# Kernel optimization log

Measured on AMD Instinct MI355X. Metric: run time of the kernel, lower is better.

The kernel has to match this reference:

```python
import jax, jax.numpy as jnp
import numpy as np

N_NODES = 100000
N_EDGES = 800000
IN_DIM, HID, OUT_DIM = 128, 96, 32
BN_EPS = 1e-5


def gcn_conv(x, W, b, src, dst, n):
    # PyG GCNConv: linear -> symmetric-normalized aggregation (with self-loops) -> +bias
    h = x @ W  # [N, out]
    sl = jnp.arange(n)
    s = jnp.concatenate([src, sl])
    d = jnp.concatenate([dst, sl])
    deg = jax.ops.segment_sum(jnp.ones(s.shape[0], dtype=x.dtype), d, num_segments=n)
    dinv = jnp.where(deg > 0, jax.lax.rsqrt(deg), 0.0)
    norm = dinv[s] * dinv[d]  # [E+N]
    out = jax.ops.segment_sum(norm[:, None] * h[s], d, num_segments=n)
    return out + b


def batchnorm(x, gamma, beta):
    mu = jnp.mean(x, axis=0)
    var = jnp.var(x, axis=0)
    return gamma * (x - mu) * jax.lax.rsqrt(var + BN_EPS) + beta


def setup_inputs() -> dict:
    key = jax.random.key(0)
    ks = jax.random.split(key, 8)
    glorot = lambda k, fi, fo: jax.random.normal(k, (fi, fo), jnp.float32) * np.sqrt(2.0 / (fi + fo))
    return {
        "x": jax.random.normal(ks[0], (N_NODES, IN_DIM), jnp.float32),
        "edge_index": jax.random.randint(ks[1], (2, N_EDGES), 0, N_NODES, jnp.int64),
        "W1": glorot(ks[2], IN_DIM, HID), "b1": jnp.zeros((HID,), jnp.float32),
        "W2": glorot(ks[3], HID, HID), "b2": jnp.zeros((HID,), jnp.float32),
        "W3": glorot(ks[4], HID, OUT_DIM), "b3": jnp.zeros((OUT_DIM,), jnp.float32),
        "g1": jnp.ones((HID,), jnp.float32), "be1": jnp.zeros((HID,), jnp.float32),
        "g2": jnp.ones((HID,), jnp.float32), "be2": jnp.zeros((HID,), jnp.float32),
    }


def reference(x, edge_index, W1, b1, W2, b2, W3, b3, g1, be1, g2, be2):
    src, dst = edge_index[0], edge_index[1]
    n = x.shape[0]
    h = gcn_conv(x, W1, b1, src, dst, n)
    h = jax.nn.relu(batchnorm(h, g1, be1))  # dropout is identity in eval
    h = gcn_conv(h, W2, b2, src, dst, n)
    h = jax.nn.relu(batchnorm(h, g2, be2))
    h = gcn_conv(h, W3, b3, src, dst, n)
    return jax.nn.log_softmax(h, axis=-1)
```

## Files before the change

### kernel.cpp

```cpp
#include <hip/hip_runtime.h>
#include <hip/hip_fp16.h>
#include <cstddef>

#define NN 100000
#define NE 800000
#define DIN 128
#define HID 96
#define DOUT 32
static constexpr float BN_EPS = 1e-5f;
#define SCAN_NB ((NN + 255) / 256)

typedef unsigned short u16;
typedef unsigned int u32;

__device__ __forceinline__ float b2f(u32 lo16) {
    union { u32 u; float f; } c; c.u = lo16 << 16; return c.f;
}
__device__ __forceinline__ u16 f2b(float f) {
    union { float f; u32 u; } c; c.f = f;
    return (u16)((c.u + 0x7FFFu + ((c.u >> 16) & 1u)) >> 16);
}
__device__ __forceinline__ u32 pack_edge(int s, float w) {
    __half h = __float2half(w);
    return ((u32)s << 15) | (u32)__half_as_ushort(h);
}
__device__ __forceinline__ int edge_src(u32 pk) { return (int)(pk >> 15); }
__device__ __forceinline__ float edge_wt(u32 pk) {
    return __half2float(__ushort_as_half((u16)(pk & 0x7FFFu)));
}


__global__ void k_init(int* __restrict__ deg) {
    int i = blockIdx.x * 256 + threadIdx.x;
    if (i < NN) deg[i] = 0;
}

__global__ __launch_bounds__(256) void k_scan1(const int* __restrict__ deg,
                                               int* __restrict__ row_start,
                                               int* __restrict__ blksum,
                                               float* __restrict__ dinv) {
    __shared__ int lds[256];
    int t = threadIdx.x;
    int i = blockIdx.x * 256 + t;
    int v = (i < NN) ? deg[i] : 0;
    if (i < NN) dinv[i] = rsqrtf((float)(v + 1));
    lds[t] = v;
    __syncthreads();
#pragma unroll
    for (int off = 1; off < 256; off <<= 1) {
        int add = (t >= off) ? lds[t - off] : 0;
        __syncthreads();
        lds[t] += add;
        __syncthreads();
    }
    if (i < NN) row_start[i] = lds[t] - v;
    if (t == 255) blksum[blockIdx.x] = lds[255];
}

__global__ __launch_bounds__(512) void k_scan2(int* __restrict__ blksum,
                                               int* __restrict__ row_start,
                                               float* __restrict__ meta) {
    __shared__ int lds[512];
    int t = threadIdx.x;
    if (t < 384) meta[t] = 0.f;
    int v = (t < SCAN_NB) ? blksum[t] : 0;
    lds[t] = v;
    __syncthreads();
#pragma unroll
    for (int off = 1; off < 512; off <<= 1) {
        int add = (t >= off) ? lds[t - off] : 0;
        __syncthreads();
        lds[t] += add;
        __syncthreads();
    }
    if (t < SCAN_NB) blksum[t] = lds[t] - v;
    if (t == 511) row_start[NN] = lds[511];
}

__global__ __launch_bounds__(256) void k_scan3(int* __restrict__ row_start,
                                               const int* __restrict__ blksum) {
    int i = blockIdx.x * 256 + threadIdx.x;
    if (i < NN) row_start[i] += blksum[blockIdx.x];
}

__global__ void k_scatter(const int* __restrict__ src, const int* __restrict__ dst,
                          const int* __restrict__ row_start,
                          const int* __restrict__ rank,
                          const float* __restrict__ dinv,
                          u32* __restrict__ ewt) {
    int e = blockIdx.x * blockDim.x + threadIdx.x;
    if (e < NE) {
        int d = dst[e];
        int p = row_start[d] + rank[e];
        int s = src[e];
        ewt[p] = pack_edge(s, dinv[s]);
    }
}

template <int KD, int ND, bool FUSE, typename XT>
__device__ __forceinline__ void gemm_body(int bid, const XT* __restrict__ X,
                                          const float* __restrict__ W,
                                          u16* __restrict__ Z,
                                          const float* __restrict__ bnA,
                                          const float* __restrict__ bnC, int M) {
    constexpr int BK = 32;
    constexpr int CT = 16;
    constexpr int CPT = ND / CT;
    constexpr int RPT = 8;
    constexpr int XS = 132;
    __shared__ float Xs[BK * XS];
    __shared__ float Ws[BK * ND];
    __shared__ float As[KD], Cs[KD];

    int tid = threadIdx.x;
    if (FUSE && tid < KD) { As[tid] = bnA[tid]; Cs[tid] = bnC[tid]; }
    int row0 = bid * 128;
    int ct = tid % CT, rt = tid / CT;
    float acc[RPT][CPT];
#pragma unroll
    for (int r = 0; r < RPT; ++r)
#pragma unroll
        for (int c = 0; c < CPT; ++c) acc[r][c] = 0.f;

    for (int k0 = 0; k0 < KD; k0 += BK) {
        __syncthreads();
        if constexpr (sizeof(XT) == 4) {
#pragma unroll
            for (int pass = 0; pass < 4; ++pass) {
                int r = pass * 32 + (tid >> 3);
                int kq = (tid & 7) * 4;
                int grow = row0 + r;
                float4 v = make_float4(0.f, 0.f, 0.f, 0.f);
                if (grow < M) v = *(const float4*)&X[(size_t)grow * KD + k0 + kq];
                if (FUSE) {
                    v.x = fmaxf(fmaf(As[k0 + kq + 0], v.x, Cs[k0 + kq + 0]), 0.f);
                    v.y = fmaxf(fmaf(As[k0 + kq + 1], v.y, Cs[k0 + kq + 1]), 0.f);
                    v.z = fmaxf(fmaf(As[k0 + kq + 2], v.z, Cs[k0 + kq + 2]), 0.f);
                    v.w = fmaxf(fmaf(As[k0 + kq + 3], v.w, Cs[k0 + kq + 3]), 0.f);
                }
                Xs[(kq + 0) * XS + r] = v.x;
                Xs[(kq + 1) * XS + r] = v.y;
                Xs[(kq + 2) * XS + r] = v.z;
                Xs[(kq + 3) * XS + r] = v.w;
            }
        } else {
#pragma unroll
            for (int pass = 0; pass < 2; ++pass) {
                int r = pass * 64 + (tid >> 2);
                int kq = (tid & 3) * 8;
                int grow = row0 + r;
                uint4 v = make_uint4(0, 0, 0, 0);
                if (grow < M) v = *(const uint4*)&X[(size_t)grow * KD + k0 + kq];
                u32 w[4] = {v.x, v.y, v.z, v.w};
#pragma unroll
                for (int q = 0; q < 4; ++q) {
                    float lo = b2f(w[q] & 0xFFFFu);
                    float hi = b2f(w[q] >> 16);
                    if (FUSE) {
                        lo = fmaxf(fmaf(As[k0 + kq + 2 * q + 0], lo, Cs[k0 + kq + 2 * q + 0]), 0.f);
                        hi = fmaxf(fmaf(As[k0 + kq + 2 * q + 1], hi, Cs[k0 + kq + 2 * q + 1]), 0.f);
                    }
                    Xs[(kq + 2 * q + 0) * XS + r] = lo;
                    Xs[(kq + 2 * q + 1) * XS + r] = hi;
                }
            }
        }
#pragma unroll
        for (int f = tid; f < BK * ND / 4; f += 256) {
            int kk = f / (ND / 4);
            int c4 = (f % (ND / 4)) * 4;
            *(float4*)&Ws[kk * ND + c4] = *(const float4*)&W[(size_t)(k0 + kk) * ND + c4];
        }
        __syncthreads();
#pragma unroll
        for (int kk = 0; kk < BK; ++kk) {
            float4 x0 = *(const float4*)&Xs[kk * XS + rt * 8];
            float4 x1 = *(const float4*)&Xs[kk * XS + rt * 8 + 4];
            float xr[RPT] = {x0.x, x0.y, x0.z, x0.w, x1.x, x1.y, x1.z, x1.w};
            float wc[CPT];
#pragma unroll
            for (int c = 0; c < CPT; ++c) wc[c] = Ws[kk * ND + ct * CPT + c];
#pragma unroll
            for (int r = 0; r < RPT; ++r)
#pragma unroll
                for (int c = 0; c < CPT; ++c) acc[r][c] = fmaf(xr[r], wc[c], acc[r][c]);
        }
    }
#pragma unroll
    for (int r = 0; r < RPT; ++r) {
        int grow = row0 + rt * RPT + r;
        if (grow < M) {
#pragma unroll
            for (int c = 0; c < CPT; c += 2) {
                u32 pk = (u32)f2b(acc[r][c]) | ((u32)f2b(acc[r][c + 1]) << 16);
                *(u32*)&Z[(size_t)grow * ND + ct * CPT + c] = pk;
            }
        }
    }
}

template <int KD, int ND, bool FUSE, typename XT>
__global__ __launch_bounds__(256) void k_gemm(const XT* __restrict__ X,
                                              const float* __restrict__ W,
                                              u16* __restrict__ Z,
                                              const float* __restrict__ bnA,
                                              const float* __restrict__ bnC, int M) {
    gemm_body<KD, ND, FUSE, XT>(blockIdx.x, X, W, Z, bnA, bnC, M);
}

__global__ __launch_bounds__(256) void k_gemm1_hist(const float* __restrict__ X,
                                                    const float* __restrict__ W,
                                                    u16* __restrict__ Z, int M,
                                                    int gemm_blocks,
                                                    const int* __restrict__ dst,
                                                    int* __restrict__ deg,
                                                    int* __restrict__ rank) {
    if ((int)blockIdx.x < gemm_blocks) {
        gemm_body<DIN, HID, false, float>(blockIdx.x, X, W, Z, nullptr, nullptr, M);
    } else {
        int e = ((int)blockIdx.x - gemm_blocks) * 256 + (int)threadIdx.x;
        if (e < NE) rank[e] = atomicAdd(&deg[dst[e]], 1);
    }
}

__global__ __launch_bounds__(256) void k_agg96(const u16* __restrict__ Z,
                                               u16* __restrict__ H,
                                               const float* __restrict__ bias,
                                               const int* __restrict__ row_start,
                                               const u32* __restrict__ ewt,
                                               const float* __restrict__ dinv,
                                               float* __restrict__ gsum,
                                               float* __restrict__ gsq) {
    __shared__ float ssum[96], ssq[96];
    int tid = threadIdx.x;
    if (tid < 96) { ssum[tid] = 0.f; ssq[tid] = 0.f; }
    __syncthreads();
    int wid = tid >> 6, lane = tid & 63;
    bool act = lane < 48;
    int l = act ? lane : 47;
    const u32* zu = (const u32*)Z;
    float b0 = bias[2 * l], b1 = bias[2 * l + 1];
    float lsum0 = 0.f, lsq0 = 0.f, lsum1 = 0.f, lsq1 = 0.f;
    const int stride = gridDim.x * 4;

    int n = blockIdx.x * 4 + wid;
    int e0 = 0, e1 = 0;
    u32 pr = 0;
    if (n < NN) {
        e0 = row_start[n]; e1 = row_start[n + 1];
        if (e0 + lane < e1) pr = ewt[e0 + lane];
    }
    while (n < NN) {
        int n2 = n + stride;
        int e0n = 0, e1n = 0;
        if (n2 < NN) { e0n = row_start[n2]; e1n = row_start[n2 + 1]; }

        float dn = dinv[n];
        u32 uself = zu[(size_t)n * 48 + l];
        float a0a = dn * b2f(uself & 0xFFFFu);
        float a1a = dn * b2f(uself >> 16);
        float a0b = 0.f, a1b = 0.f;

        u32 plv = pr;

        u32 prn = 0;
        if (n2 < NN && e0n + lane < e1n) prn = ewt[e0n + lane];

        int m = e1 - e0;
        if (m <= 64) {
            int K = (m + 7) >> 3;
            u32 uA[8], uB[8];
            float wA[8], wB[8];
            {
#pragma unroll
                for (int q = 0; q < 8; ++q) {
                    bool v = q < m;
                    u32 pk = __shfl(plv, v ? q : 0);
                    wA[q] = v ? edge_wt(pk) : 0.f;
                    uA[q] = zu[(size_t)edge_src(pk) * 48 + l];
                }
            }
            for (int c = 0; c < K; ++c) {
                if ((c & 1) == 0) {
                    if (c + 1 < K) {
#pragma unroll
                        for (int q = 0; q < 8; ++q) {
                            int j = (c + 1) * 8 + q;
                            bool v = j < m;
                            u32 pk = __shfl(plv, v ? j : 0);
                            wB[q] = v ? edge_wt(pk) : 0.f;
                            uB[q] = zu[(size_t)edge_src(pk) * 48 + l];
                        }
                    }
#pragma unroll
                    for (int q = 0; q < 8; q += 2) {
                        a0a = fmaf(wA[q], b2f(uA[q] & 0xFFFFu), a0a);
                        a1a = fmaf(wA[q], b2f(uA[q] >> 16), a1a);
                        a0b = fmaf(wA[q + 1], b2f(uA[q + 1] & 0xFFFFu), a0b);
                        a1b = fmaf(wA[q + 1], b2f(uA[q + 1] >> 16), a1b);
                    }
                } else {
                    if (c + 1 < K) {
#pragma unroll
                        for (int q = 0; q < 8; ++q) {
                            int j = (c + 1) * 8 + q;
                            bool v = j < m;
                            u32 pk = __shfl(plv, v ? j : 0);
                            wA[q] = v ? edge_wt(pk) : 0.f;
                            uA[q] = zu[(size_t)edge_src(pk) * 48 + l];
                        }
                    }
#pragma unroll
                    for (int q = 0; q < 8; q += 2) {
                        a0a = fmaf(wB[q], b2f(uB[q] & 0xFFFFu), a0a);
                        a1a = fmaf(wB[q], b2f(uB[q] >> 16), a1a);
                        a0b = fmaf(wB[q + 1], b2f(uB[q + 1] & 0xFFFFu), a0b);
                        a1b = fmaf(wB[q + 1], b2f(uB[q + 1] >> 16), a1b);
                    }
                }
            }
        } else {
            u32 cw = plv;
            for (int eb = e0; eb < e1; eb += 64) {
                if (eb != e0) {
                    int idx = eb + lane;
                    cw = (idx < e1) ? ewt[idx] : 0;
                }
                int mm = e1 - eb; if (mm > 64) mm = 64;
                for (int j = 0; j < mm; ++j) {
                    u32 pk = __shfl(cw, j);
                    float w = edge_wt(pk);
                    u32 u = zu[(size_t)edge_src(pk) * 48 + l];
                    a0a = fmaf(w, b2f(u & 0xFFFFu), a0a);
                    a1a = fmaf(w, b2f(u >> 16), a1a);
                }
            }
        }
        float h0 = fmaf(dn, a0a + a0b, b0);
        float h1 = fmaf(dn, a1a + a1b, b1);
        if (act) {
            u32 pk = (u32)f2b(h0) | ((u32)f2b(h1) << 16);
            ((u32*)H)[(size_t)n * 48 + l] = pk;
            lsum0 += h0; lsq0 = fmaf(h0, h0, lsq0);
            lsum1 += h1; lsq1 = fmaf(h1, h1, lsq1);
        }
        n = n2; e0 = e0n; e1 = e1n; pr = prn;
    }
    if (act) {
        atomicAdd(&ssum[2 * l], lsum0); atomicAdd(&ssq[2 * l], lsq0);
        atomicAdd(&ssum[2 * l + 1], lsum1); atomicAdd(&ssq[2 * l + 1], lsq1);
    }
    __syncthreads();
    if (tid < 96) { atomicAdd(&gsum[tid], ssum[tid]); atomicAdd(&gsq[tid], ssq[tid]); }
}

__global__ void k_bncoef(const float* __restrict__ gsum, const float* __restrict__ gsq,
                         const float* __restrict__ g, const float* __restrict__ be,
                         float* __restrict__ bnA, float* __restrict__ bnC) {
    int c = threadIdx.x;
    if (c < 96) {
        float mean = gsum[c] * (1.f / NN);
        float var = gsq[c] * (1.f / NN) - mean * mean;
        float inv = rsqrtf(var + BN_EPS);
        float a = g[c] * inv;
        bnA[c] = a;
        bnC[c] = fmaf(-a, mean, be[c]);
    }
}

__global__ __launch_bounds__(256) void k_agg32_lsm(const u16* __restrict__ Z,
                                                   float* __restrict__ Out,
                                                   const float* __restrict__ bias,
                                                   const int* __restrict__ row_start,
                                                   const u32* __restrict__ ewt,
                                                   const float* __restrict__ dinv) {
    int tid = threadIdx.x;
    int wid = tid >> 6, lane = tid & 63;
    int g = lane >> 4, sl = lane & 15;
    const u32* zu = (const u32*)Z;
    float b0 = bias[2 * sl], b1 = bias[2 * sl + 1];
    int stride = gridDim.x * 16;
    for (int n0 = (blockIdx.x * 4 + wid) * 4; n0 < NN; n0 += stride) {
        int n = n0 + g;
        bool vn = n < NN;
        float dn = vn ? dinv[n] : 0.f;
        u32 uself = vn ? zu[(size_t)n * 16 + sl] : 0;
        float a0a = dn * b2f(uself & 0xFFFFu);
        float a1a = dn * b2f(uself >> 16);
        float a0b = 0.f, a1b = 0.f;
        int e0 = vn ? row_start[n] : 0, e1 = vn ? row_start[n + 1] : 0;
        for (int eb = e0; eb < e1; eb += 16) {
            int m = e1 - eb; if (m > 16) m = 16;
            int idx = eb + sl;
            u32 plv = (idx < e1) ? ewt[idx] : 0;
            u32 u_[16]; float w_[16];
#pragma unroll
            for (int q = 0; q < 16; ++q) {
                bool v = q < m;
                u32 pk = __shfl(plv, v ? q : 0, 16);
                w_[q] = v ? edge_wt(pk) : 0.f;
                u_[q] = zu[(size_t)edge_src(pk) * 16 + sl];
            }
#pragma unroll
            for (int q = 0; q < 16; q += 2) {
                a0a = fmaf(w_[q], b2f(u_[q] & 0xFFFFu), a0a);
                a1a = fmaf(w_[q], b2f(u_[q] >> 16), a1a);
                a0b = fmaf(w_[q + 1], b2f(u_[q + 1] & 0xFFFFu), a0b);
                a1b = fmaf(w_[q + 1], b2f(u_[q + 1] >> 16), a1b);
            }
        }
        float v0 = fmaf(dn, a0a + a0b, b0);
        float v1 = fmaf(dn, a1a + a1b, b1);
        float mx = fmaxf(v0, v1);
#pragma unroll
        for (int off = 8; off; off >>= 1) mx = fmaxf(mx, __shfl_xor(mx, off, 16));
        float ex = __expf(v0 - mx) + __expf(v1 - mx);
#pragma unroll
        for (int off = 8; off; off >>= 1) ex += __shfl_xor(ex, off, 16);
        float lse = mx + __logf(ex);
        if (vn) {
            float2 o = make_float2(v0 - lse, v1 - lse);
            *(float2*)&Out[(size_t)n * 32 + 2 * sl] = o;
        }
    }
}


extern "C" void kernel_launch(void* const* d_in, const int* in_sizes, int n_in,
                              void* d_out, int out_size, void* d_ws, size_t ws_size,
                              hipStream_t stream) {
    const float* x  = (const float*)d_in[0];
    const int* ei   = (const int*)d_in[1];
    const float* W1 = (const float*)d_in[2];
    const float* b1 = (const float*)d_in[3];
    const float* W2 = (const float*)d_in[4];
    const float* b2 = (const float*)d_in[5];
    const float* W3 = (const float*)d_in[6];
    const float* b3 = (const float*)d_in[7];
    const float* g1 = (const float*)d_in[8];
    const float* be1 = (const float*)d_in[9];
    const float* g2 = (const float*)d_in[10];
    const float* be2 = (const float*)d_in[11];
    float* out = (float*)d_out;

    const int* src = ei;
    const int* dst = ei + NE;

    char* p = (char*)d_ws;
    size_t off = 0;
    auto take = [&](size_t bytes) {
        char* r = p + off;
        off = (off + bytes + 255) & ~(size_t)255;
        return r;
    };
    float* dinv      = (float*)take(NN * 4);
    int*   deg       = (int*)take(NN * 4);
    int*   row_start = (int*)take((NN + 1) * 4);
    int*   blksum    = (int*)take(SCAN_NB * 4);
    int*   rank      = (int*)take((size_t)NE * 4);
    u32*   ewt       = (u32*)take((size_t)NE * 4);
    float* meta      = (float*)take(768 * 4);
    u16*   bufA      = (u16*)take((size_t)NN * HID * 2);
    u16*   bufB      = (u16*)take((size_t)NN * HID * 2);

    float* sum1 = meta + 0,   *sq1 = meta + 96;
    float* sum2 = meta + 192, *sq2 = meta + 288;
    float* bnA1 = meta + 384, *bnC1 = meta + 480;
    float* bnA2 = meta + 576, *bnC2 = meta + 672;

    const int EB = (NE + 255) / 256;
    const int VB = (NN + 255) / 256;
    const int GB = (NN + 127) / 128;
    const int AB = 2048;

    k_init<<<VB, 256, 0, stream>>>(deg);
    k_gemm1_hist<<<GB + EB, 256, 0, stream>>>(x, W1, bufA, NN, GB, dst, deg, rank);
    k_scan1<<<SCAN_NB, 256, 0, stream>>>(deg, row_start, blksum, dinv);
    k_scan2<<<1, 512, 0, stream>>>(blksum, row_start, meta);
    k_scan3<<<SCAN_NB, 256, 0, stream>>>(row_start, blksum);
    k_scatter<<<EB, 256, 0, stream>>>(src, dst, row_start, rank, dinv, ewt);

    k_agg96<<<AB, 256, 0, stream>>>(bufA, bufB, b1, row_start, ewt, dinv, sum1, sq1);
    k_bncoef<<<1, 128, 0, stream>>>(sum1, sq1, g1, be1, bnA1, bnC1);

    k_gemm<HID, HID, true, u16><<<GB, 256, 0, stream>>>(bufB, W2, bufA, bnA1, bnC1, NN);
    k_agg96<<<AB, 256, 0, stream>>>(bufA, bufB, b2, row_start, ewt, dinv, sum2, sq2);
    k_bncoef<<<1, 128, 0, stream>>>(sum2, sq2, g2, be2, bnA2, bnC2);

    k_gemm<HID, DOUT, true, u16><<<GB, 256, 0, stream>>>(bufB, W3, bufA, bnA2, bnC2, NN);
    k_agg32_lsm<<<AB, 256, 0, stream>>>(bufA, out, b3, row_start, ewt, dinv);

    (void)in_sizes; (void)n_in; (void)out_size; (void)ws_size;
}
```

Before: 436.1 us.

## Software-pipeline GCN aggregation across nodes with 16-edge gather prefetch

Restructures the 96-wide aggregation kernel into a multi-stage pipeline. Row bounds are fetched three nodes ahead, edge words two nodes ahead, and up to 16 neighbor feature rows for the next node are gathered while the current node is accumulated, using double-buffered register arrays. Edge counts are made wave-uniform with readfirstlane, and addressing uses 32-bit byte offsets. The aim is to hide gather latency across node iterations, at the cost of higher register pressure. Nodes with more than 16 edges now do the remaining gathers serially with no prefetch.

```diff
diff --git a/kernel.cpp b/kernel.cpp
--- a/kernel.cpp
+++ b/kernel.cpp
@@ -27,6 +27,9 @@
 __device__ __forceinline__ int edge_src(u32 pk) { return (int)(pk >> 15); }
 __device__ __forceinline__ float edge_wt(u32 pk) {
     return __half2float(__ushort_as_half((u16)(pk & 0x7FFFu)));
+}
+__device__ __forceinline__ u32 ld32(const u32* __restrict__ base, u32 byteoff) {
+    return *(const u32*)((const char*)base + byteoff);
 }
 
 
@@ -238,114 +241,124 @@
     int wid = tid >> 6, lane = tid & 63;
     bool act = lane < 48;
     int l = act ? lane : 47;
+    u32 l4 = (u32)l << 2;
     const u32* zu = (const u32*)Z;
     float b0 = bias[2 * l], b1 = bias[2 * l + 1];
     float lsum0 = 0.f, lsq0 = 0.f, lsum1 = 0.f, lsq1 = 0.f;
-    const int stride = gridDim.x * 4;
-
-    int n = blockIdx.x * 4 + wid;
-    int e0 = 0, e1 = 0;
-    u32 pr = 0;
-    if (n < NN) {
-        e0 = row_start[n]; e1 = row_start[n + 1];
-        if (e0 + lane < e1) pr = ewt[e0 + lane];
-    }
-    while (n < NN) {
-        int n2 = n + stride;
-        int e0n = 0, e1n = 0;
-        if (n2 < NN) { e0n = row_start[n2]; e1n = row_start[n2 + 1]; }
-
-        float dn = dinv[n];
-        u32 uself = zu[(size_t)n * 48 + l];
-        float a0a = dn * b2f(uself & 0xFFFFu);
-        float a1a = dn * b2f(uself >> 16);
+    const int S = gridDim.x * 4;
+
+    int nA = blockIdx.x * 4 + wid;
+    int nB = nA + S, nC = nB + S, nD = nC + S;
+    int e0A = 0, e1A = 0, e0B = 0, e1B = 0, e0C = 0, e1C = 0;
+    u32 prA = 0, prB = 0;
+    u32 selfA = 0, selfB = 0;
+    float dnA = 0.f, dnB = 0.f;
+    u32 uA[16], uB[16];
+    u32 prC_ = 0; int e0D_ = 0, e1D_ = 0;
+
+    auto prefetch_rows = [&](u32 (&dst)[16], u32 pr, int m) {
+#pragma unroll
+        for (int q = 0; q < 16; ++q) {
+            if (q < m) {
+                u32 pk = __shfl(pr, q);
+                dst[q] = ld32(zu, (u32)edge_src(pk) * 192u + l4);
+            }
+        }
+    };
+
+    e0A = row_start[nA]; e1A = row_start[nA + 1];
+    if (nB < NN) { e0B = row_start[nB]; e1B = row_start[nB + 1]; }
+    if (nC < NN) { e0C = row_start[nC]; e1C = row_start[nC + 1]; }
+    if (e0A + lane < e1A) prA = ewt[e0A + lane];
+    if (nB < NN && e0B + lane < e1B) prB = ewt[e0B + lane];
+    dnA = dinv[nA];
+    selfA = ld32(zu, (u32)nA * 192u + l4);
+    prefetch_rows(uA, prA, __builtin_amdgcn_readfirstlane(e1A - e0A));
+
+    auto stage = [&](u32 (&uNxt)[16]) {
+        if (nB < NN) {
+            dnB = dinv[nB];
+            selfB = ld32(zu, (u32)nB * 192u + l4);
+            prefetch_rows(uNxt, prB, __builtin_amdgcn_readfirstlane(e1B - e0B));
+        }
+        prC_ = 0;
+        if (nC < NN && e0C + lane < e1C) prC_ = ewt[e0C + lane];
+        e0D_ = 0; e1D_ = 0;
+        if (nD < NN) { e0D_ = row_start[nD]; e1D_ = row_start[nD + 1]; }
+    };
+
+    auto compute = [&](u32 (&u)[16]) {
+        int e0s = __builtin_amdgcn_readfirstlane(e0A);
+        int e1s = __builtin_amdgcn_readfirstlane(e1A);
+        int m = e1s - e0s;
+        float a0a = dnA * b2f(selfA & 0xFFFFu);
+        float a1a = dnA * b2f(selfA >> 16);
         float a0b = 0.f, a1b = 0.f;
-
-        u32 plv = pr;
-
-        u32 prn = 0;
-        if (n2 < NN && e0n + lane < e1n) prn = ewt[e0n + lane];
-
-        int m = e1 - e0;
-        if (m <= 64) {
-            int K = (m + 7) >> 3;
-            u32 uA[8], uB[8];
-            float wA[8], wB[8];
-            {
-#pragma unroll
-                for (int q = 0; q < 8; ++q) {
-                    bool v = q < m;
-                    u32 pk = __shfl(plv, v ? q : 0);
-                    wA[q] = v ? edge_wt(pk) : 0.f;
-                    uA[q] = zu[(size_t)edge_src(pk) * 48 + l];
-                }
-            }
-            for (int c = 0; c < K; ++c) {
-                if ((c & 1) == 0) {
-                    if (c + 1 < K) {
-#pragma unroll
-                        for (int q = 0; q < 8; ++q) {
-                            int j = (c + 1) * 8 + q;
-                            bool v = j < m;
-                            u32 pk = __shfl(plv, v ? j : 0);
-                            wB[q] = v ? edge_wt(pk) : 0.f;
-                            uB[q] = zu[(size_t)edge_src(pk) * 48 + l];
-                        }
-                    }
-#pragma unroll
-                    for (int q = 0; q < 8; q += 2) {
-                        a0a = fmaf(wA[q], b2f(uA[q] & 0xFFFFu), a0a);
-                        a1a = fmaf(wA[q], b2f(uA[q] >> 16), a1a);
-                        a0b = fmaf(wA[q + 1], b2f(uA[q + 1] & 0xFFFFu), a0b);
-                        a1b = fmaf(wA[q + 1], b2f(uA[q + 1] >> 16), a1b);
-                    }
-                } else {
-                    if (c + 1 < K) {
-#pragma unroll
-                        for (int q = 0; q < 8; ++q) {
-                            int j = (c + 1) * 8 + q;
-                            bool v = j < m;
-                            u32 pk = __shfl(plv, v ? j : 0);
-                            wA[q] = v ? edge_wt(pk) : 0.f;
-                            uA[q] = zu[(size_t)edge_src(pk) * 48 + l];
-                        }
-                    }
-#pragma unroll
-                    for (int q = 0; q < 8; q += 2) {
-                        a0a = fmaf(wB[q], b2f(uB[q] & 0xFFFFu), a0a);
-                        a1a = fmaf(wB[q], b2f(uB[q] >> 16), a1a);
-                        a0b = fmaf(wB[q + 1], b2f(uB[q + 1] & 0xFFFFu), a0b);
-                        a1b = fmaf(wB[q + 1], b2f(uB[q + 1] >> 16), a1b);
-                    }
-                }
-            }
-        } else {
-            u32 cw = plv;
-            for (int eb = e0; eb < e1; eb += 64) {
-                if (eb != e0) {
-                    int idx = eb + lane;
-                    cw = (idx < e1) ? ewt[idx] : 0;
-                }
-                int mm = e1 - eb; if (mm > 64) mm = 64;
+#pragma unroll
+        for (int q = 0; q < 16; q += 2) {
+            if (q < m) {
+                u32 pk = __shfl(prA, q);
+                float w = edge_wt(pk);
+                a0a = fmaf(w, b2f(u[q] & 0xFFFFu), a0a);
+                a1a = fmaf(w, b2f(u[q] >> 16), a1a);
+            }
+            if (q + 1 < m) {
+                u32 pk = __shfl(prA, q + 1);
+                float w = edge_wt(pk);
+                a0b = fmaf(w, b2f(u[q + 1] & 0xFFFFu), a0b);
+                a1b = fmaf(w, b2f(u[q + 1] >> 16), a1b);
+            }
+        }
+        if (m > 16) {
+            int lim = m < 64 ? m : 64;
+            for (int j = 16; j < lim; ++j) {
+                u32 pk = __shfl(prA, j);
+                float w = edge_wt(pk);
+                u32 uu = ld32(zu, (u32)edge_src(pk) * 192u + l4);
+                a0a = fmaf(w, b2f(uu & 0xFFFFu), a0a);
+                a1a = fmaf(w, b2f(uu >> 16), a1a);
+            }
+            for (int eb = e0s + 64; eb < e1s; eb += 64) {
+                int idx = eb + lane;
+                u32 cw = (idx < e1s) ? ewt[idx] : 0;
+                int mm = e1s - eb; if (mm > 64) mm = 64;
                 for (int j = 0; j < mm; ++j) {
                     u32 pk = __shfl(cw, j);
                     float w = edge_wt(pk);
-                    u32 u = zu[(size_t)edge_src(pk) * 48 + l];
-                    a0a = fmaf(w, b2f(u & 0xFFFFu), a0a);
-                    a1a = fmaf(w, b2f(u >> 16), a1a);
+                    u32 uu = ld32(zu, (u32)edge_src(pk) * 192u + l4);
+                    a0a = fmaf(w, b2f(uu & 0xFFFFu), a0a);
+                    a1a = fmaf(w, b2f(uu >> 16), a1a);
                 }
             }
         }
-        float h0 = fmaf(dn, a0a + a0b, b0);
-        float h1 = fmaf(dn, a1a + a1b, b1);
+        float h0 = fmaf(dnA, a0a + a0b, b0);
+        float h1 = fmaf(dnA, a1a + a1b, b1);
         if (act) {
             u32 pk = (u32)f2b(h0) | ((u32)f2b(h1) << 16);
-            ((u32*)H)[(size_t)n * 48 + l] = pk;
+            ((u32*)H)[(size_t)nA * 48 + l] = pk;
             lsum0 += h0; lsq0 = fmaf(h0, h0, lsq0);
             lsum1 += h1; lsq1 = fmaf(h1, h1, lsq1);
         }
-        n = n2; e0 = e0n; e1 = e1n; pr = prn;
-    }
+    };
+
+#define AGG_ROT()                                                        \
+    nA = nB; e0A = e0B; e1A = e1B; prA = prB; dnA = dnB; selfA = selfB;  \
+    nB = nC; e0B = e0C; e1B = e1C; prB = prC_;                           \
+    nC = nD; e0C = e0D_; e1C = e1D_;                                     \
+    nD += S
+
+    for (;;) {
+        stage(uB);
+        compute(uA);
+        AGG_ROT();
+        if (nA >= NN) break;
+        stage(uA);
+        compute(uB);
+        AGG_ROT();
+        if (nA >= NN) break;
+    }
+#undef AGG_ROT
+
     if (act) {
         atomicAdd(&ssum[2 * l], lsum0); atomicAdd(&ssq[2 * l], lsq0);
         atomicAdd(&ssum[2 * l + 1], lsum1); atomicAdd(&ssq[2 * l + 1], lsq1);
```

Result: no change. 438.7 us (+0.6%).

## Gather 16-byte feature chunks with four edges per wavefront in agg96

Applied to the files above, without the earlier changes.

Restructures the 96-wide aggregation so each wavefront splits into four 16-lane groups. Each group handles a different edge and loads 8 bf16 features per lane with a uint4 load. The groups' partial sums are then reduced with cross-lane shuffles. This replaces 4-byte per-lane gathers, where 16 of 64 lanes sat idle, with wider vector loads and more edges in flight. In exchange it adds shuffle reductions, more registers for the 8 accumulators, and a smaller unrolled prefetch window for nodes with up to 16 edges.

```diff
diff --git a/kernel.cpp b/kernel.cpp
--- a/kernel.cpp
+++ b/kernel.cpp
@@ -223,6 +223,16 @@
     }
 }
 
+#define ACC8(UB, W)                                                     \
+    acc[0] = fmaf(W, b2f((UB).x & 0xFFFFu), acc[0]);                    \
+    acc[1] = fmaf(W, b2f((UB).x >> 16), acc[1]);                        \
+    acc[2] = fmaf(W, b2f((UB).y & 0xFFFFu), acc[2]);                    \
+    acc[3] = fmaf(W, b2f((UB).y >> 16), acc[3]);                        \
+    acc[4] = fmaf(W, b2f((UB).z & 0xFFFFu), acc[4]);                    \
+    acc[5] = fmaf(W, b2f((UB).z >> 16), acc[5]);                        \
+    acc[6] = fmaf(W, b2f((UB).w & 0xFFFFu), acc[6]);                    \
+    acc[7] = fmaf(W, b2f((UB).w >> 16), acc[7]);
+
 __global__ __launch_bounds__(256) void k_agg96(const u16* __restrict__ Z,
                                                u16* __restrict__ H,
                                                const float* __restrict__ bias,
@@ -236,12 +246,19 @@
     if (tid < 96) { ssum[tid] = 0.f; ssq[tid] = 0.f; }
     __syncthreads();
     int wid = tid >> 6, lane = tid & 63;
-    bool act = lane < 48;
-    int l = act ? lane : 47;
-    const u32* zu = (const u32*)Z;
-    float b0 = bias[2 * l], b1 = bias[2 * l + 1];
-    float lsum0 = 0.f, lsq0 = 0.f, lsum1 = 0.f, lsq1 = 0.f;
-    const int stride = gridDim.x * 4;
+    int r = lane >> 4;
+    int jraw = lane & 15;
+    int j = jraw < 12 ? jraw : 11;
+    bool jact = jraw < 12;
+    u32 j16 = (u32)j << 4;
+    const char* zb = (const char*)Z;
+    float bia[8];
+#pragma unroll
+    for (int k = 0; k < 8; ++k) bia[k] = bias[8 * j + k];
+    float lsum[8], lsq[8];
+#pragma unroll
+    for (int k = 0; k < 8; ++k) { lsum[k] = 0.f; lsq[k] = 0.f; }
+    const int S = gridDim.x * 4;
 
     int n = blockIdx.x * 4 + wid;
     int e0 = 0, e1 = 0;
@@ -251,104 +268,91 @@
         if (e0 + lane < e1) pr = ewt[e0 + lane];
     }
     while (n < NN) {
-        int n2 = n + stride;
+        int n2 = n + S;
         int e0n = 0, e1n = 0;
         if (n2 < NN) { e0n = row_start[n2]; e1n = row_start[n2 + 1]; }
-
-        float dn = dinv[n];
-        u32 uself = zu[(size_t)n * 48 + l];
-        float a0a = dn * b2f(uself & 0xFFFFu);
-        float a1a = dn * b2f(uself >> 16);
-        float a0b = 0.f, a1b = 0.f;
-
-        u32 plv = pr;
-
         u32 prn = 0;
         if (n2 < NN && e0n + lane < e1n) prn = ewt[e0n + lane];
 
+        float dn = dinv[n];
         int m = e1 - e0;
-        if (m <= 64) {
-            int K = (m + 7) >> 3;
-            u32 uA[8], uB[8];
-            float wA[8], wB[8];
-            {
-#pragma unroll
-                for (int q = 0; q < 8; ++q) {
-                    bool v = q < m;
-                    u32 pk = __shfl(plv, v ? q : 0);
-                    wA[q] = v ? edge_wt(pk) : 0.f;
-                    uA[q] = zu[(size_t)edge_src(pk) * 48 + l];
+        float acc[8];
+        uint4 us4 = make_uint4(0, 0, 0, 0);
+        if (r == 0) us4 = *(const uint4*)(zb + (u32)n * 192u + j16);
+        if (r == 0) {
+            acc[0] = dn * b2f(us4.x & 0xFFFFu); acc[1] = dn * b2f(us4.x >> 16);
+            acc[2] = dn * b2f(us4.y & 0xFFFFu); acc[3] = dn * b2f(us4.y >> 16);
+            acc[4] = dn * b2f(us4.z & 0xFFFFu); acc[5] = dn * b2f(us4.z >> 16);
+            acc[6] = dn * b2f(us4.w & 0xFFFFu); acc[7] = dn * b2f(us4.w >> 16);
+        } else {
+#pragma unroll
+            for (int k = 0; k < 8; ++k) acc[k] = 0.f;
+        }
+
+        if (m <= 16) {
+            uint4 ub[4]; float wc[4];
+            int nch = (m + 3) >> 2;
+#pragma unroll
+            for (int c = 0; c < 4; ++c) {
+                if (c < nch) {
+                    int e = 4 * c + r;
+                    u32 pk = __shfl(pr, e < m ? e : 0);
+                    wc[c] = (e < m) ? edge_wt(pk) : 0.f;
+                    ub[c] = *(const uint4*)(zb + (pk >> 15) * 192u + j16);
                 }
             }
-            for (int c = 0; c < K; ++c) {
-                if ((c & 1) == 0) {
-                    if (c + 1 < K) {
-#pragma unroll
-                        for (int q = 0; q < 8; ++q) {
-                            int j = (c + 1) * 8 + q;
-                            bool v = j < m;
-                            u32 pk = __shfl(plv, v ? j : 0);
-                            wB[q] = v ? edge_wt(pk) : 0.f;
-                            uB[q] = zu[(size_t)edge_src(pk) * 48 + l];
-                        }
-                    }
-#pragma unroll
-                    for (int q = 0; q < 8; q += 2) {
-                        a0a = fmaf(wA[q], b2f(uA[q] & 0xFFFFu), a0a);
-                        a1a = fmaf(wA[q], b2f(uA[q] >> 16), a1a);
-                        a0b = fmaf(wA[q + 1], b2f(uA[q + 1] & 0xFFFFu), a0b);
-                        a1b = fmaf(wA[q + 1], b2f(uA[q + 1] >> 16), a1b);
-                    }
-                } else {
-                    if (c + 1 < K) {
-#pragma unroll
-                        for (int q = 0; q < 8; ++q) {
-                            int j = (c + 1) * 8 + q;
-                            bool v = j < m;
-                            u32 pk = __shfl(plv, v ? j : 0);
-                            wA[q] = v ? edge_wt(pk) : 0.f;
-                            uA[q] = zu[(size_t)edge_src(pk) * 48 + l];
-                        }
-                    }
-#pragma unroll
-                    for (int q = 0; q < 8; q += 2) {
-                        a0a = fmaf(wB[q], b2f(uB[q] & 0xFFFFu), a0a);
-                        a1a = fmaf(wB[q], b2f(uB[q] >> 16), a1a);
-                        a0b = fmaf(wB[q + 1], b2f(uB[q + 1] & 0xFFFFu), a0b);
-                        a1b = fmaf(wB[q + 1], b2f(uB[q + 1] >> 16), a1b);
-                    }
-                }
+#pragma unroll
+            for (int c = 0; c < 4; ++c) {
+                if (c < nch) { ACC8(ub[c], wc[c]); }
             }
         } else {
-            u32 cw = plv;
-            for (int eb = e0; eb < e1; eb += 64) {
-                if (eb != e0) {
-                    int idx = eb + lane;
+            for (int base = 0; base < m; base += 64) {
+                u32 cw = pr;
+                if (base) {
+                    int idx = e0 + base + lane;
                     cw = (idx < e1) ? ewt[idx] : 0;
                 }
-                int mm = e1 - eb; if (mm > 64) mm = 64;
-                for (int j = 0; j < mm; ++j) {
-                    u32 pk = __shfl(cw, j);
-                    float w = edge_wt(pk);
-                    u32 u = zu[(size_t)edge_src(pk) * 48 + l];
-                    a0a = fmaf(w, b2f(u & 0xFFFFu), a0a);
-                    a1a = fmaf(w, b2f(u >> 16), a1a);
+                int lim = m - base; if (lim > 64) lim = 64;
+                for (int c = 0; c < lim; c += 4) {
+                    int e = c + r;
+                    u32 pk = __shfl(cw, e < lim ? e : 0);
+                    float w = (e < lim) ? edge_wt(pk) : 0.f;
+                    uint4 ub = *(const uint4*)(zb + (pk >> 15) * 192u + j16);
+                    ACC8(ub, w);
                 }
             }
         }
-        float h0 = fmaf(dn, a0a + a0b, b0);
-        float h1 = fmaf(dn, a1a + a1b, b1);
-        if (act) {
-            u32 pk = (u32)f2b(h0) | ((u32)f2b(h1) << 16);
-            ((u32*)H)[(size_t)n * 48 + l] = pk;
-            lsum0 += h0; lsq0 = fmaf(h0, h0, lsq0);
-            lsum1 += h1; lsq1 = fmaf(h1, h1, lsq1);
+
+#pragma unroll
+        for (int k = 0; k < 8; ++k) {
+            float v = acc[k];
+            v += __shfl_xor(v, 16);
+            v += __shfl_xor(v, 32);
+            acc[k] = v;
+        }
+        if (r == 0 && jact) {
+            float h[8];
+#pragma unroll
+            for (int k = 0; k < 8; ++k) {
+                h[k] = fmaf(dn, acc[k], bia[k]);
+                lsum[k] += h[k];
+                lsq[k] = fmaf(h[k], h[k], lsq[k]);
+            }
+            uint4 o;
+            o.x = (u32)f2b(h[0]) | ((u32)f2b(h[1]) << 16);
+            o.y = (u32)f2b(h[2]) | ((u32)f2b(h[3]) << 16);
+            o.z = (u32)f2b(h[4]) | ((u32)f2b(h[5]) << 16);
+            o.w = (u32)f2b(h[6]) | ((u32)f2b(h[7]) << 16);
+            *(uint4*)((char*)H + (u32)n * 192u + j16) = o;
         }
         n = n2; e0 = e0n; e1 = e1n; pr = prn;
     }
-    if (act) {
-        atomicAdd(&ssum[2 * l], lsum0); atomicAdd(&ssq[2 * l], lsq0);
-        atomicAdd(&ssum[2 * l + 1], lsum1); atomicAdd(&ssq[2 * l + 1], lsq1);
+    if (r == 0 && jact) {
+#pragma unroll
+        for (int k = 0; k < 8; ++k) {
+            atomicAdd(&ssum[8 * j + k], lsum[k]);
+            atomicAdd(&ssq[8 * j + k], lsq[k]);
+        }
     }
     __syncthreads();
     if (tid < 96) { atomicAdd(&gsum[tid], ssum[tid]); atomicAdd(&gsq[tid], ssq[tid]); }
```

After: 422.6 us. -3.1%, faster.
